# Kernel optimization log

Measured on AMD Instinct MI355X. Metric: run time of the kernel, lower is better.

Reference implementation:

```python
import jax, jax.numpy as jnp
import numpy as np

DIM = 128
R = 3
D = 2 * R + 1          # diameter = 7
D2 = D * D             # 49
B, H, W = 4, 64, 64
EPS_LN = 1e-6


def conv1x1(x, w, b):
    # x: [B,Cin,H,W], w: [Cout,Cin], b: [Cout]
    return jnp.einsum('oi,bihw->bohw', w, x) + b[None, :, None, None]


def ln2d(x, w, b):
    u = x.mean(1, keepdims=True)
    s = ((x - u) ** 2).mean(1, keepdims=True)
    xn = (x - u) / jnp.sqrt(s + EPS_LN)
    return w[None, :, None, None] * xn + b[None, :, None, None]


def extract_patches(x):
    # x: [B,C,H,W] -> [B,C,D2,H,W], n = ki*D+kj, value = padded[:, :, h+ki, w+kj]
    xp = jnp.pad(x, ((0, 0), (0, 0), (R, R), (R, R)), mode='reflect')
    Hh, Ww = x.shape[2], x.shape[3]
    return jnp.stack([xp[:, :, ki:ki + Hh, kj:kj + Ww]
                      for ki in range(D) for kj in range(D)], axis=2)


def setup_inputs() -> dict:
    key = jax.random.key(0)
    ks = jax.random.split(key, 16)
    sd = 0.02
    inp = {
        'spatial_feats': jax.random.normal(ks[0], (B, DIM, H, W), jnp.float32),
        'semantic_feats': jax.random.normal(ks[1], (B, DIM, H, W), jnp.float32),
        # range_proj: conv1x1 -> LN2d -> SiLU -> conv1x1
        'rp_w1': jax.random.normal(ks[2], (DIM, DIM), jnp.float32) * sd,
        'rp_b1': jnp.zeros((DIM,), jnp.float32),
        'rp_lnw': jnp.ones((DIM,), jnp.float32),
        'rp_lnb': jnp.zeros((DIM,), jnp.float32),
        'rp_w2': jax.random.normal(ks[3], (DIM, DIM), jnp.float32) * sd,
        'rp_b2': jnp.zeros((DIM,), jnp.float32),
        # fixup_proj: conv1x1(D2+DIM -> D2) -> LN2d -> SiLU -> conv1x1(D2 -> D2)
        'fx_w1': jax.random.normal(ks[4], (D2, D2 + DIM), jnp.float32) * sd,
        'fx_b1': jnp.zeros((D2,), jnp.float32),
        'fx_lnw': jnp.ones((D2,), jnp.float32),
        'fx_lnb': jnp.zeros((D2,), jnp.float32),
        'fx_w2': jax.random.normal(ks[5], (D2, D2), jnp.float32) * sd,
        'fx_b2': jnp.zeros((D2,), jnp.float32),
        'sigma_spatial': jnp.float32(1.0),
        # output_proj: conv1x1 -> LN2d -> conv1x1
        'op_w1': jax.random.normal(ks[6], (DIM, DIM), jnp.float32) * sd,
        'op_b1': jnp.zeros((DIM,), jnp.float32),
        'op_lnw': jnp.ones((DIM,), jnp.float32),
        'op_lnb': jnp.zeros((DIM,), jnp.float32),
        'op_w2': jax.random.normal(ks[7], (DIM, DIM), jnp.float32) * sd,
        'op_b2': jnp.zeros((DIM,), jnp.float32),
    }
    return inp


def reference(spatial_feats, semantic_feats,
              rp_w1, rp_b1, rp_lnw, rp_lnb, rp_w2, rp_b2,
              fx_w1, fx_b1, fx_lnw, fx_lnb, fx_w2, fx_b2,
              sigma_spatial,
              op_w1, op_b1, op_lnw, op_lnb, op_w2, op_b2):
    scale = DIM ** 0.5

    # range_proj (dropout is identity in eval)
    px = conv1x1(semantic_feats, rp_w1, rp_b1)
    px = jax.nn.silu(ln2d(px, rp_lnw, rp_lnb))
    proj_x = conv1x1(px, rp_w2, rp_b2)

    # spatial kernel [1, D2, 1, 1]
    dist = jnp.linspace(-1.0, 1.0, D)
    gx, gy = jnp.meshgrid(dist, dist, indexing='ij')
    spatial_kernel = jnp.exp(-(gx ** 2 + gy ** 2) /
                             (2.0 * sigma_spatial ** 2)).reshape(1, D2, 1, 1)

    # range kernel: softmax over neighborhood of <query, neighbor>/sqrt(dim)
    queries = extract_patches(proj_x)                    # [B,C,D2,H,W]
    sim = jnp.einsum('bcnhw,bchw->bnhw', queries, proj_x) / scale
    range_kernel = jax.nn.softmax(sim.astype(jnp.float32), axis=1)

    combined = range_kernel * spatial_kernel             # [B,D2,H,W]

    # fixup gating
    fx = conv1x1(jnp.concatenate([combined, semantic_feats], axis=1), fx_w1, fx_b1)
    fx = jax.nn.silu(ln2d(fx, fx_lnw, fx_lnb))
    fx = conv1x1(fx, fx_w2, fx_b2)
    combined = combined + combined * jax.nn.sigmoid(fx)
    combined = combined / (combined.sum(1, keepdims=True) + 1e-7)

    # weighted neighborhood aggregation of spatial features
    neighborhoods = extract_patches(spatial_feats)       # [B,C,D2,H,W]
    out = jnp.einsum('bcnhw,bnhw->bchw', neighborhoods, combined)

    # output_proj (no activation, dropout identity)
    out = conv1x1(out, op_w1, op_b1)
    out = ln2d(out, op_lnw, op_lnb)
    out = conv1x1(out, op_w2, op_b2)
    return out
```

## Files before the change

### kernel.cpp

```cpp
#include <hip/hip_runtime.h>
#include <cstdint>

#define BB 4
#define CDIM 128
#define HH 64
#define WW 64
#define RR 3
#define DD 7
#define DSQ 49

typedef __attribute__((ext_vector_type(8))) short short8v;
typedef __attribute__((ext_vector_type(4))) float float4v;

__device__ __forceinline__ int reflect64(int p) {
    p = (p < 0) ? -p : p;
    return (p > 63) ? (126 - p) : p;
}
__device__ __forceinline__ float sigm(float x) { return 1.0f / (1.0f + __expf(-x)); }
__device__ __forceinline__ short f2bf(float f) {
    uint32_t u = __float_as_uint(f);
    u += 0x7FFF + ((u >> 16) & 1);
    return (short)(u >> 16);
}

template<bool SILU>
__global__ __launch_bounds__(1024) void proj_kernel(
    const float* __restrict__ x, const float* __restrict__ w1,
    const float* __restrict__ b1, const float* __restrict__ lnw,
    const float* __restrict__ lnb, const float* __restrict__ w2,
    const float* __restrict__ b2, short* __restrict__ outT)
{
    __shared__ short sW1[CDIM * CDIM];
    __shared__ short sW2[CDIM * CDIM];
    __shared__ short sXT[WW * CDIM];
    __shared__ short sXT2[WW * CDIM];
    __shared__ float sT[CDIM][65];
    __shared__ float red1[16][WW];
    __shared__ float red2[16][WW];

    const int tid = threadIdx.x;
    const int l = tid & 63;
    const int q = tid >> 6;
    const int qu = __builtin_amdgcn_readfirstlane(q);
    const int b = blockIdx.x >> 6;
    const int h = blockIdx.x & 63;

    {
        const int o = tid >> 3;
        const int i0 = (tid & 7) * 16;
        const int sw = (o & 7) << 3;
        const float* wsrc[2] = {w1, w2};
        short* wdst[2] = {sW1, sW2};
        #pragma unroll
        for (int m = 0; m < 2; ++m) {
            const float* src = wsrc[m] + o * CDIM + i0;
            short8v pk0, pk1;
            #pragma unroll
            for (int j = 0; j < 8; ++j) pk0[j] = f2bf(src[j]);
            #pragma unroll
            for (int j = 0; j < 8; ++j) pk1[j] = f2bf(src[8 + j]);
            *reinterpret_cast<short8v*>(&wdst[m][o * 128 + (i0 ^ sw)]) = pk0;
            *reinterpret_cast<short8v*>(&wdst[m][o * 128 + ((i0 + 8) ^ sw)]) = pk1;
        }
    }
    {
        const int pos = tid & 15;
        const int c0 = tid >> 4;
        const float* xrow = x + (b * CDIM * HH + h) * WW;
        #pragma unroll
        for (int rr = 0; rr < 2; ++rr) {
            const int c = c0 + rr * 64;
            const float4 v = *reinterpret_cast<const float4*>(&xrow[c * HH * WW + pos * 4]);
            #pragma unroll
            for (int m = 0; m < 4; ++m) {
                const int p = pos * 4 + m;
                sXT[p * 128 + (c ^ ((p & 7) << 3))] = f2bf(((const float*)&v)[m]);
            }
        }
    }
    __syncthreads();

    const int lm = l & 15, g = l >> 4;
    const int tm = q >> 1;
    const int tn0 = (q & 1) * 2;
    const int oa = tm * 16 + lm;
    const int arow = oa * 128, asw = (oa & 7) << 3;
    const int p0 = tn0 * 16 + lm, p1 = (tn0 + 1) * 16 + lm;
    const int bsw0 = (p0 & 7) << 3, bsw1 = (p1 & 7) << 3;

    float4v acc0 = {0.f, 0.f, 0.f, 0.f}, acc1 = {0.f, 0.f, 0.f, 0.f};
    #pragma unroll
    for (int kk = 0; kk < 4; ++kk) {
        const int ki = kk * 32 + g * 8;
        const short8v af = *reinterpret_cast<const short8v*>(&sW1[arow + (ki ^ asw)]);
        const short8v bf0 = *reinterpret_cast<const short8v*>(&sXT[p0 * 128 + (ki ^ bsw0)]);
        const short8v bf1 = *reinterpret_cast<const short8v*>(&sXT[p1 * 128 + (ki ^ bsw1)]);
        acc0 = __builtin_amdgcn_mfma_f32_16x16x32_bf16(af, bf0, acc0, 0, 0, 0);
        acc1 = __builtin_amdgcn_mfma_f32_16x16x32_bf16(af, bf1, acc1, 0, 0, 0);
    }
    #pragma unroll
    for (int r = 0; r < 4; ++r) sT[tm * 16 + g * 4 + r][p0] = acc0[r];
    #pragma unroll
    for (int r = 0; r < 4; ++r) sT[tm * 16 + g * 4 + r][p1] = acc1[r];
    __syncthreads();

    {
        const int p = l;
        float vals[8];
        float s1 = 0.f, s2 = 0.f;
        #pragma unroll
        for (int j = 0; j < 8; ++j) {
            const float v = sT[qu * 8 + j][p] + b1[qu * 8 + j];
            vals[j] = v; s1 += v; s2 += v * v;
        }
        red1[q][p] = s1; red2[q][p] = s2;
        __syncthreads();
        float t1 = 0.f, t2 = 0.f;
        #pragma unroll
        for (int j = 0; j < 16; ++j) { t1 += red1[j][p]; t2 += red2[j][p]; }
        const float mean = t1 * (1.0f / 128.0f);
        const float var  = t2 * (1.0f / 128.0f) - mean * mean;
        const float rstd = rsqrtf(var + 1e-6f);
        short8v pk;
        #pragma unroll
        for (int j = 0; j < 8; ++j) {
            float v = (vals[j] - mean) * rstd * lnw[qu * 8 + j] + lnb[qu * 8 + j];
            if (SILU) v = v * sigm(v);
            pk[j] = f2bf(v);
        }
        *reinterpret_cast<short8v*>(&sXT2[p * 128 + ((qu * 8) ^ ((p & 7) << 3))]) = pk;
    }
    __syncthreads();

    {
        float4v a0 = {0.f, 0.f, 0.f, 0.f}, a1 = {0.f, 0.f, 0.f, 0.f};
        #pragma unroll
        for (int kk = 0; kk < 4; ++kk) {
            const int ki = kk * 32 + g * 8;
            const short8v af = *reinterpret_cast<const short8v*>(&sW2[arow + (ki ^ asw)]);
            const short8v bf0 = *reinterpret_cast<const short8v*>(&sXT2[p0 * 128 + (ki ^ bsw0)]);
            const short8v bf1 = *reinterpret_cast<const short8v*>(&sXT2[p1 * 128 + (ki ^ bsw1)]);
            a0 = __builtin_amdgcn_mfma_f32_16x16x32_bf16(af, bf0, a0, 0, 0, 0);
            a1 = __builtin_amdgcn_mfma_f32_16x16x32_bf16(af, bf1, a1, 0, 0, 0);
        }
        const float4 bv = *reinterpret_cast<const float4*>(&b2[tm * 16 + g * 4]);
        #pragma unroll
        for (int r = 0; r < 4; ++r) {
            const float bias = ((const float*)&bv)[r];
            sT[tm * 16 + g * 4 + r][p0] = a0[r] + bias;
            sT[tm * 16 + g * 4 + r][p1] = a1[r] + bias;
        }
    }
    __syncthreads();
    {
        const int p = tid >> 4;
        const int c0 = (tid & 15) * 8;
        short8v pk;
        #pragma unroll
        for (int j = 0; j < 8; ++j) pk[j] = f2bf(sT[c0 + j][p]);
        *reinterpret_cast<short8v*>(&outT[((b * HH + h) * WW + p) * CDIM + c0]) = pk;
    }
}

__global__ __launch_bounds__(1024) void simfixagg_kernel(
    const short* __restrict__ pxt, const float* __restrict__ sigma_p,
    const float* __restrict__ sem,
    const float* __restrict__ fw1, const float* __restrict__ fb1,
    const float* __restrict__ flnw, const float* __restrict__ flnb,
    const float* __restrict__ fw2, const float* __restrict__ fb2,
    const float* __restrict__ spatial,
    const float* __restrict__ ow1, const float* __restrict__ ob1,
    const float* __restrict__ olnw, const float* __restrict__ olnb,
    const float* __restrict__ ow2, const float* __restrict__ ob2,
    float* __restrict__ out)
{
    __shared__ alignas(16) char sBig[7 * WW * CDIM * 2];
    __shared__ alignas(16) char sAux[64 * 66 * 4];
    __shared__ alignas(16) float sSimWts[DSQ][64];
    __shared__ alignas(16) float sCmb[DSQ][66];

    short* rows = reinterpret_cast<short*>(sBig);
    short* B1   = reinterpret_cast<short*>(sBig);
    short* A1   = reinterpret_cast<short*>(sBig + 24576);
    short* B2   = reinterpret_cast<short*>(sBig + 49152);
    short* A2   = reinterpret_cast<short*>(sBig + 57344);
    float* fSem = reinterpret_cast<float*>(sBig + 65536);
    float* prm  = reinterpret_cast<float*>(sBig + 98304);
    short* W0   = reinterpret_cast<short*>(sBig);
    short* W1   = reinterpret_cast<short*>(sBig + 9216);
    short* sSa  = reinterpret_cast<short*>(sBig + 18432);
    float (*sT)[65] = reinterpret_cast<float(*)[65]>(sBig);
    short* sWb  = reinterpret_cast<short*>(sBig + 57344);
    short* sXT  = reinterpret_cast<short*>(sBig + 90112);

    float (*sP64)[66] = reinterpret_cast<float(*)[66]>(sAux);
    float (*red1)[65] = reinterpret_cast<float(*)[65]>(sAux);
    float (*red2)[65] = reinterpret_cast<float(*)[65]>(sAux + 16 * 65 * 4);

    const int tid = threadIdx.x;
    const int l = tid & 63;
    const int q = tid >> 6;
    const int qu = __builtin_amdgcn_readfirstlane(q);
    const int lbid = ((blockIdx.x & 7) << 5) | (blockIdx.x >> 3);
    const int b = lbid >> 6;
    const int h = lbid & 63;

    for (int idx = tid; idx < 7 * WW * 16; idx += 1024) {
        const int cchunk = idx & 15;
        const int p = (idx >> 4) & 63;
        const int row = idx >> 10;
        const int hp = reflect64(h + row - RR);
        const short8v v = *reinterpret_cast<const short8v*>(
            &pxt[((b * HH + hp) * WW + p) * CDIM + cchunk * 8]);
        *reinterpret_cast<short8v*>(
            &rows[(row * WW + p) * CDIM + ((cchunk * 8) ^ ((p & 7) << 3))]) = v;
    }
    __syncthreads();

    const int lm = l & 15, g = l >> 4;
    const int tm = q >> 2, tn = q & 3;
    const int pa = tm * 16 + lm;
    const int pxb = tn * 16 + lm;
    const int abase = (3 * WW + pa) * CDIM, as_ = (pa & 7) << 3;
    const int bs_ = (pxb & 7) << 3;

    short8v afr[4];
    #pragma unroll
    for (int kk = 0; kk < 4; ++kk)
        afr[kk] = *reinterpret_cast<const short8v*>(
            &rows[abase + ((kk * 32 + g * 8) ^ as_)]);

    const float rscale = 0.088388347648318447f;
    for (int ki = 0; ki < 7; ++ki) {
        float4v acc = {0.f, 0.f, 0.f, 0.f};
        const int bbase = (ki * WW + pxb) * CDIM;
        #pragma unroll
        for (int kk = 0; kk < 4; ++kk) {
            const short8v bf = *reinterpret_cast<const short8v*>(
                &rows[bbase + ((kk * 32 + g * 8) ^ bs_)]);
            acc = __builtin_amdgcn_mfma_f32_16x16x32_bf16(afr[kk], bf, acc, 0, 0, 0);
        }
        #pragma unroll
        for (int r = 0; r < 4; ++r)
            sP64[tm * 16 + g * 4 + r][tn * 16 + lm] = acc[r];
        __syncthreads();
        if (tid < 448) {
            const int kj = tid >> 6, p = tid & 63;
            sSimWts[ki * 7 + kj][p] = sP64[p][reflect64(p + kj - RR)] * rscale;
        }
        __syncthreads();
    }

    for (int idx = tid; idx < 64 * 24; idx += 1024) {
        const int o = idx / 24;
        const int ch0 = (idx % 24) * 8;
        short8v pk;
        #pragma unroll
        for (int j = 0; j < 8; ++j) {
            const int c = ch0 + j;
            float v = 0.f;
            if (o < DSQ) {
                if (c < DSQ) v = fw1[o * 177 + c];
                else if (c >= 64) v = fw1[o * 177 + DSQ + (c - 64)];
            }
            pk[j] = f2bf(v);
        }
        *reinterpret_cast<short8v*>(&A1[o * 192 + (ch0 ^ ((o & 7) << 3))]) = pk;
    }
    for (int idx = tid; idx < 64 * 8; idx += 1024) {
        const int o = idx >> 3;
        const int ch0 = (idx & 7) * 8;
        short8v pk;
        #pragma unroll
        for (int j = 0; j < 8; ++j) {
            const int c = ch0 + j;
            pk[j] = (o < DSQ && c < DSQ) ? f2bf(fw2[o * DSQ + c]) : (short)0;
        }
        *reinterpret_cast<short8v*>(&A2[o * 64 + (ch0 ^ ((o & 7) << 3))]) = pk;
    }
    {
        const short8v z = {0, 0, 0, 0, 0, 0, 0, 0};
        for (int idx = tid; idx < 64 * 8; idx += 1024)
            *reinterpret_cast<short8v*>(&B2[idx * 8]) = z;
    }
    for (int idx = tid; idx < 64 * 15; idx += 1024) {
        const int p = idx / 15, c = DSQ + idx % 15;
        B1[p * 192 + (c ^ ((p & 7) << 3))] = 0;
    }
    for (int idx = tid; idx < 256; idx += 1024) {
        const int a = idx >> 6, i = idx & 63;
        float v = 0.f;
        if (i < DSQ) {
            if (a == 0) v = fb1[i];
            else if (a == 1) v = flnw[i];
            else if (a == 2) v = flnb[i];
            else v = fb2[i];
        }
        prm[a * 64 + i] = v;
    }
    {
        const float* srow = sem + (b * CDIM * HH + h) * WW;
        for (int idx = tid; idx < CDIM * 16; idx += 1024) {
            const int r = idx >> 4, pos = idx & 15;
            *reinterpret_cast<float4*>(&fSem[r * WW + pos * 4]) =
                *reinterpret_cast<const float4*>(&srow[r * HH * WW + pos * 4]);
        }
    }
    {
        float rv[DSQ];
        #pragma unroll
        for (int n = 0; n < DSQ; ++n) rv[n] = sSimWts[n][l];
        float m = -1e30f;
        #pragma unroll
        for (int n = 0; n < DSQ; ++n) m = fmaxf(m, rv[n]);
        float ssum = 0.f;
        #pragma unroll
        for (int n = 0; n < DSQ; ++n) ssum += __expf(rv[n] - m);
        const float inv = 1.0f / ssum;
        const float sigma = sigma_p[0];
        const float inv2s2 = 1.0f / (2.0f * sigma * sigma);
        const int swl = (l & 7) << 3;
        #pragma unroll
        for (int k = 0; k < 4; ++k) {
            const int n = q + 16 * k;
            if (n < DSQ) {
                const int ki = n / 7, kj = n % 7;
                const float dx = (float)(ki - 3) * (1.0f / 3.0f);
                const float dy = (float)(kj - 3) * (1.0f / 3.0f);
                const float sk = __expf(-(dx * dx + dy * dy) * inv2s2);
                const float cv = __expf(rv[n] - m) * inv * sk;
                sCmb[n][l] = cv;
                B1[l * 192 + (n ^ swl)] = f2bf(cv);
            }
        }
    }
    __syncthreads();
    {
        const int c0 = q * 8;
        short8v pk;
        #pragma unroll
        for (int j = 0; j < 8; ++j) pk[j] = f2bf(fSem[(c0 + j) * WW + l]);
        *reinterpret_cast<short8v*>(&B1[l * 192 + ((64 + c0) ^ ((l & 7) << 3))]) = pk;
    }
    __syncthreads();

    const int oA = tm * 16 + lm;
    const int aswz = (oA & 7) << 3;
    const int p = tn * 16 + lm;
    const int bswz = (p & 7) << 3;

    float4v facc = {0.f, 0.f, 0.f, 0.f};
    #pragma unroll
    for (int kk = 0; kk < 6; ++kk) {
        const int ki = kk * 32 + g * 8;
        const short8v af = *reinterpret_cast<const short8v*>(&A1[oA * 192 + (ki ^ aswz)]);
        const short8v bf = *reinterpret_cast<const short8v*>(&B1[p * 192 + (ki ^ bswz)]);
        facc = __builtin_amdgcn_mfma_f32_16x16x32_bf16(af, bf, facc, 0, 0, 0);
    }
    float vals[4];
    float s1 = 0.f, s2 = 0.f;
    #pragma unroll
    for (int r = 0; r < 4; ++r) {
        const int o = tm * 16 + g * 4 + r;
        const float v = facc[r] + prm[o];
        vals[r] = v;
        if (o < DSQ) { s1 += v; s2 += v * v; }
    }
    red1[tm * 4 + g][p] = s1;
    red2[tm * 4 + g][p] = s2;
    __syncthreads();
    float t1 = 0.f, t2 = 0.f;
    #pragma unroll
    for (int j = 0; j < 16; ++j) { t1 += red1[j][p]; t2 += red2[j][p]; }
    const float mean = t1 * (1.0f / 49.0f);
    const float var  = t2 * (1.0f / 49.0f) - mean * mean;
    const float rstd = rsqrtf(var + 1e-6f);
    #pragma unroll
    for (int r = 0; r < 4; ++r) {
        const int o = tm * 16 + g * 4 + r;
        if (o < DSQ) {
            const float v = (vals[r] - mean) * rstd * prm[64 + o] + prm[128 + o];
            const float sv = v * sigm(v);
            B2[p * 64 + (o ^ bswz)] = f2bf(sv);
        }
    }
    __syncthreads();

    float4v facc2 = {0.f, 0.f, 0.f, 0.f};
    #pragma unroll
    for (int kk = 0; kk < 2; ++kk) {
        const int ki = kk * 32 + g * 8;
        const short8v af = *reinterpret_cast<const short8v*>(&A2[oA * 64 + (ki ^ aswz)]);
        const short8v bf = *reinterpret_cast<const short8v*>(&B2[p * 64 + (ki ^ bswz)]);
        facc2 = __builtin_amdgcn_mfma_f32_16x16x32_bf16(af, bf, facc2, 0, 0, 0);
    }
    float c2v[4];
    float ps = 0.f;
    #pragma unroll
    for (int r = 0; r < 4; ++r) {
        const int o = tm * 16 + g * 4 + r;
        if (o < DSQ) {
            const float f = facc2[r] + prm[192 + o];
            c2v[r] = sCmb[o][p] * (1.0f + sigm(f));
            ps += c2v[r];
        } else c2v[r] = 0.f;
    }
    red1[tm * 4 + g][p] = ps;
    __syncthreads();
    float tot = 0.f;
    #pragma unroll
    for (int j = 0; j < 16; ++j) tot += red1[j][p];
    const float invt = 1.0f / (tot + 1e-7f);
    #pragma unroll
    for (int r = 0; r < 4; ++r) {
        const int o = tm * 16 + g * 4 + r;
        if (o < DSQ) sSimWts[o][p] = c2v[r] * invt;
    }
    __syncthreads();

    {
        const int o = tid >> 3;
        const int i0 = (tid & 7) * 16;
        const int sw = (o & 7) << 3;
        const float* src = ow1 + o * CDIM + i0;
        short8v pk0, pk1;
        #pragma unroll
        for (int j = 0; j < 8; ++j) pk0[j] = f2bf(src[j]);
        #pragma unroll
        for (int j = 0; j < 8; ++j) pk1[j] = f2bf(src[8 + j]);
        *reinterpret_cast<short8v*>(&sWb[o * 128 + (i0 ^ sw)]) = pk0;
        *reinterpret_cast<short8v*>(&sWb[o * 128 + ((i0 + 8) ^ sw)]) = pk1;
    }

    const float* sb = spatial + b * CDIM * HH * WW;
    float4 sreg[2];
    #define LD_SROW(KI)                                                          \
        { const int hp_ = reflect64(h + (KI) - RR);                              \
          _Pragma("unroll")                                                      \
          for (int j = 0; j < 2; ++j) {                                          \
              const int idx = tid * 2 + j;                                       \
              const int c = idx >> 4, pos = idx & 15;                            \
              sreg[j] = *reinterpret_cast<const float4*>(                        \
                  &sb[(c * HH + hp_) * WW + pos * 4]);                           \
          } }
    #define ST_SROW()                                                            \
        { _Pragma("unroll")                                                      \
          for (int j = 0; j < 2; ++j) {                                          \
              const int idx = tid * 2 + j;                                       \
              const int c = idx >> 4, pos = idx & 15;                            \
              const int sw_ = (c & 7) << 3;                                      \
              _Pragma("unroll")                                                  \
              for (int m = 0; m < 4; ++m)                                        \
                  sSa[c * 64 + ((pos * 4 + m) ^ sw_)] =                          \
                      f2bf(((const float*)&sreg[j])[m]);                         \
          } }
    #define ZERO_W(DST)                                                          \
        { const short8v z8 = {0,0,0,0,0,0,0,0};                                  \
          if (tid < 576) *reinterpret_cast<short8v*>(&(DST)[tid * 8]) = z8; }
    #define SCATTER_W(DST, KIN)                                                  \
        if (tid < 64) {                                                          \
            const int pp_ = tid;                                                 \
            const int s_ = (pp_ > 3) ? (pp_ - 3) : 0;                            \
            float col[7] = {0.f, 0.f, 0.f, 0.f, 0.f, 0.f, 0.f};                  \
            _Pragma("unroll")                                                    \
            for (int kj = 0; kj < 7; ++kj) {                                     \
                const int pr = reflect64(pp_ + kj - RR);                         \
                const float wv_ = sSimWts[(KIN) * 7 + kj][pp_];                  \
                const int id_ = pr - s_;                                         \
                _Pragma("unroll")                                                \
                for (int jj = 0; jj < 7; ++jj) if (id_ == jj) col[jj] += wv_;    \
            }                                                                    \
            _Pragma("unroll")                                                    \
            for (int jj = 0; jj < 7; ++jj) {                                     \
                const int pr = s_ + jj;                                          \
                if (pr < 64) (DST)[pp_ * 72 + pr] = f2bf(col[jj]);               \
            }                                                                    \
        }

    ZERO_W(W0);
    ZERO_W(W1);
    LD_SROW(0);
    __syncthreads();
    SCATTER_W(W0, 0);
    ST_SROW();
    __syncthreads();

    const int tmA = q >> 1;
    const int oaA = tmA * 16 + lm;
    const int arA = oaA * 64, aswA = (oaA & 7) << 3;
    const int pA0 = ((q & 1) * 2) * 16 + lm, pA1 = ((q & 1) * 2 + 1) * 16 + lm;

    float4v ag0 = {0.f, 0.f, 0.f, 0.f}, ag1 = {0.f, 0.f, 0.f, 0.f};
    for (int ki = 0; ki < 7; ++ki) {
        if (ki < 6) LD_SROW(ki + 1);
        const short* Wc = (ki & 1) ? W1 : W0;
        #pragma unroll
        for (int kk = 0; kk < 2; ++kk) {
            const int k0 = kk * 32 + g * 8;
            const short8v a8 = *reinterpret_cast<const short8v*>(&sSa[arA + (k0 ^ aswA)]);
            const short8v b80 = *reinterpret_cast<const short8v*>(&Wc[pA0 * 72 + k0]);
            const short8v b81 = *reinterpret_cast<const short8v*>(&Wc[pA1 * 72 + k0]);
            ag0 = __builtin_amdgcn_mfma_f32_16x16x32_bf16(a8, b80, ag0, 0, 0, 0);
            ag1 = __builtin_amdgcn_mfma_f32_16x16x32_bf16(a8, b81, ag1, 0, 0, 0);
        }
        if (ki < 6) { SCATTER_W(((ki & 1) ? W0 : W1), ki + 1); }
        __syncthreads();
        if (ki < 6) {
            ST_SROW();
            if (ki & 1) { ZERO_W(W1); } else { ZERO_W(W0); }
            __syncthreads();
        }
    }
    #undef LD_SROW
    #undef ST_SROW
    #undef ZERO_W
    #undef SCATTER_W

    {
        #pragma unroll
        for (int r = 0; r < 4; ++r) {
            const int c = tmA * 16 + g * 4 + r;
            sXT[pA0 * 128 + (c ^ ((pA0 & 7) << 3))] = f2bf(ag0[r]);
            sXT[pA1 * 128 + (c ^ ((pA1 & 7) << 3))] = f2bf(ag1[r]);
        }
    }
    __syncthreads();

    const int tmo = q >> 1;
    const int tn0 = (q & 1) * 2;
    const int oaop = tmo * 16 + lm;
    const int arow = oaop * 128, asw = (oaop & 7) << 3;
    const int p0 = tn0 * 16 + lm, p1 = (tn0 + 1) * 16 + lm;
    const int bsw0 = (p0 & 7) << 3, bsw1 = (p1 & 7) << 3;

    {
        float4v a0 = {0.f, 0.f, 0.f, 0.f}, a1 = {0.f, 0.f, 0.f, 0.f};
        #pragma unroll
        for (int kk = 0; kk < 4; ++kk) {
            const int ki = kk * 32 + g * 8;
            const short8v af = *reinterpret_cast<const short8v*>(&sWb[arow + (ki ^ asw)]);
            const short8v bf0 = *reinterpret_cast<const short8v*>(&sXT[p0 * 128 + (ki ^ bsw0)]);
            const short8v bf1 = *reinterpret_cast<const short8v*>(&sXT[p1 * 128 + (ki ^ bsw1)]);
            a0 = __builtin_amdgcn_mfma_f32_16x16x32_bf16(af, bf0, a0, 0, 0, 0);
            a1 = __builtin_amdgcn_mfma_f32_16x16x32_bf16(af, bf1, a1, 0, 0, 0);
        }
        __syncthreads();
        #pragma unroll
        for (int r = 0; r < 4; ++r) sT[tmo * 16 + g * 4 + r][p0] = a0[r];
        #pragma unroll
        for (int r = 0; r < 4; ++r) sT[tmo * 16 + g * 4 + r][p1] = a1[r];
    }
    __syncthreads();

    {
        const int o = tid >> 3;
        const int i0 = (tid & 7) * 16;
        const int sw = (o & 7) << 3;
        const float* src = ow2 + o * CDIM + i0;
        short8v pk0, pk1;
        #pragma unroll
        for (int j = 0; j < 8; ++j) pk0[j] = f2bf(src[j]);
        #pragma unroll
        for (int j = 0; j < 8; ++j) pk1[j] = f2bf(src[8 + j]);
        *reinterpret_cast<short8v*>(&sWb[o * 128 + (i0 ^ sw)]) = pk0;
        *reinterpret_cast<short8v*>(&sWb[o * 128 + ((i0 + 8) ^ sw)]) = pk1;
    }
    {
        float vals2[8];
        float u1 = 0.f, u2 = 0.f;
        #pragma unroll
        for (int j = 0; j < 8; ++j) {
            const float v = sT[qu * 8 + j][l] + ob1[qu * 8 + j];
            vals2[j] = v; u1 += v; u2 += v * v;
        }
        red1[q][l] = u1; red2[q][l] = u2;
        __syncthreads();
        float v1 = 0.f, v2 = 0.f;
        #pragma unroll
        for (int j = 0; j < 16; ++j) { v1 += red1[j][l]; v2 += red2[j][l]; }
        const float mn = v1 * (1.0f / 128.0f);
        const float vr = v2 * (1.0f / 128.0f) - mn * mn;
        const float rs = rsqrtf(vr + 1e-6f);
        short8v pk;
        #pragma unroll
        for (int j = 0; j < 8; ++j) {
            const float v = (vals2[j] - mn) * rs * olnw[qu * 8 + j] + olnb[qu * 8 + j];
            pk[j] = f2bf(v);
        }
        *reinterpret_cast<short8v*>(&sXT[l * 128 + ((qu * 8) ^ ((l & 7) << 3))]) = pk;
    }
    __syncthreads();

    {
        float4v a0 = {0.f, 0.f, 0.f, 0.f}, a1 = {0.f, 0.f, 0.f, 0.f};
        #pragma unroll
        for (int kk = 0; kk < 4; ++kk) {
            const int ki = kk * 32 + g * 8;
            const short8v af = *reinterpret_cast<const short8v*>(&sWb[arow + (ki ^ asw)]);
            const short8v bf0 = *reinterpret_cast<const short8v*>(&sXT[p0 * 128 + (ki ^ bsw0)]);
            const short8v bf1 = *reinterpret_cast<const short8v*>(&sXT[p1 * 128 + (ki ^ bsw1)]);
            a0 = __builtin_amdgcn_mfma_f32_16x16x32_bf16(af, bf0, a0, 0, 0, 0);
            a1 = __builtin_amdgcn_mfma_f32_16x16x32_bf16(af, bf1, a1, 0, 0, 0);
        }
        const float4 bv = *reinterpret_cast<const float4*>(&ob2[tmo * 16 + g * 4]);
        float* obase = out + (b * CDIM * HH + h) * WW;
        #pragma unroll
        for (int r = 0; r < 4; ++r) {
            const float bias = ((const float*)&bv)[r];
            obase[(tmo * 16 + g * 4 + r) * HH * WW + p0] = a0[r] + bias;
            obase[(tmo * 16 + g * 4 + r) * HH * WW + p1] = a1[r] + bias;
        }
    }
}

extern "C" void kernel_launch(void* const* d_in, const int* in_sizes, int n_in,
                              void* d_out, int out_size, void* d_ws, size_t ws_size,
                              hipStream_t stream) {
    (void)in_sizes; (void)n_in; (void)out_size; (void)ws_size;
    const float* spatial  = (const float*)d_in[0];
    const float* semantic = (const float*)d_in[1];
    const float* rp_w1 = (const float*)d_in[2];
    const float* rp_b1 = (const float*)d_in[3];
    const float* rp_lnw = (const float*)d_in[4];
    const float* rp_lnb = (const float*)d_in[5];
    const float* rp_w2 = (const float*)d_in[6];
    const float* rp_b2 = (const float*)d_in[7];
    const float* fx_w1 = (const float*)d_in[8];
    const float* fx_b1 = (const float*)d_in[9];
    const float* fx_lnw = (const float*)d_in[10];
    const float* fx_lnb = (const float*)d_in[11];
    const float* fx_w2 = (const float*)d_in[12];
    const float* fx_b2 = (const float*)d_in[13];
    const float* sigma = (const float*)d_in[14];
    const float* op_w1 = (const float*)d_in[15];
    const float* op_b1 = (const float*)d_in[16];
    const float* op_lnw = (const float*)d_in[17];
    const float* op_lnb = (const float*)d_in[18];
    const float* op_w2 = (const float*)d_in[19];
    const float* op_b2 = (const float*)d_in[20];

    char* wsb = (char*)d_ws;
    short* pxt  = (short*)wsb;
    float* outp = (float*)d_out;

    dim3 grid(BB * HH), blk(1024);
    proj_kernel<true><<<grid, blk, 0, stream>>>(semantic, rp_w1, rp_b1, rp_lnw, rp_lnb,
                                                rp_w2, rp_b2, pxt);
    simfixagg_kernel<<<grid, blk, 0, stream>>>(pxt, sigma, semantic,
                                               fx_w1, fx_b1, fx_lnw, fx_lnb, fx_w2, fx_b2,
                                               spatial,
                                               op_w1, op_b1, op_lnw, op_lnb, op_w2, op_b2,
                                               outp);
}
```

Before: 54.43 us.

## Precompute all seven aggregation weight rows and double-buffer spatial rows

Builds all seven banded weight matrices at once with 448 threads before the aggregation loop, instead of scattering one per iteration with 64 threads. Spatial rows are double-buffered so each loop iteration needs one barrier instead of two. Row stores become vectorised 4-short writes. The output-projection weight load moves after the aggregation to free shared memory. This costs more shared-memory layout pressure and adds one up-front step where 448 threads zero and fill the weight rows.

```diff
diff --git a/kernel.cpp b/kernel.cpp
--- a/kernel.cpp
+++ b/kernel.cpp
@@ -10,6 +10,7 @@
 #define DSQ 49
 
 typedef __attribute__((ext_vector_type(8))) short short8v;
+typedef __attribute__((ext_vector_type(4))) short short4v;
 typedef __attribute__((ext_vector_type(4))) float float4v;
 
 __device__ __forceinline__ int reflect64(int p) {
@@ -186,12 +187,12 @@
     short* A2   = reinterpret_cast<short*>(sBig + 57344);
     float* fSem = reinterpret_cast<float*>(sBig + 65536);
     float* prm  = reinterpret_cast<float*>(sBig + 98304);
-    short* W0   = reinterpret_cast<short*>(sBig);
-    short* W1   = reinterpret_cast<short*>(sBig + 9216);
-    short* sSa  = reinterpret_cast<short*>(sBig + 18432);
-    float (*sT)[65] = reinterpret_cast<float(*)[65]>(sBig);
-    short* sWb  = reinterpret_cast<short*>(sBig + 57344);
-    short* sXT  = reinterpret_cast<short*>(sBig + 90112);
+    short* W7   = reinterpret_cast<short*>(sBig);
+    short* sSa0 = reinterpret_cast<short*>(sBig + 64512);
+    short* sSa1 = reinterpret_cast<short*>(sBig + 80896);
+    short* sWb  = reinterpret_cast<short*>(sBig);
+    short* sXT  = reinterpret_cast<short*>(sBig + 32768);
+    float (*sT)[65] = reinterpret_cast<float(*)[65]>(sBig + 49152);
 
     float (*sP64)[66] = reinterpret_cast<float(*)[66]>(sAux);
     float (*red1)[65] = reinterpret_cast<float(*)[65]>(sAux);
@@ -418,20 +419,6 @@
     }
     __syncthreads();
 
-    {
-        const int o = tid >> 3;
-        const int i0 = (tid & 7) * 16;
-        const int sw = (o & 7) << 3;
-        const float* src = ow1 + o * CDIM + i0;
-        short8v pk0, pk1;
-        #pragma unroll
-        for (int j = 0; j < 8; ++j) pk0[j] = f2bf(src[j]);
-        #pragma unroll
-        for (int j = 0; j < 8; ++j) pk1[j] = f2bf(src[8 + j]);
-        *reinterpret_cast<short8v*>(&sWb[o * 128 + (i0 ^ sw)]) = pk0;
-        *reinterpret_cast<short8v*>(&sWb[o * 128 + ((i0 + 8) ^ sw)]) = pk1;
-    }
-
     const float* sb = spatial + b * CDIM * HH * WW;
     float4 sreg[2];
     #define LD_SROW(KI)                                                          \
@@ -443,46 +430,43 @@
               sreg[j] = *reinterpret_cast<const float4*>(                        \
                   &sb[(c * HH + hp_) * WW + pos * 4]);                           \
           } }
-    #define ST_SROW()                                                            \
+    #define ST_SROW(DST)                                                         \
         { _Pragma("unroll")                                                      \
           for (int j = 0; j < 2; ++j) {                                          \
               const int idx = tid * 2 + j;                                       \
               const int c = idx >> 4, pos = idx & 15;                            \
               const int sw_ = (c & 7) << 3;                                      \
+              short4v pk;                                                        \
               _Pragma("unroll")                                                  \
-              for (int m = 0; m < 4; ++m)                                        \
-                  sSa[c * 64 + ((pos * 4 + m) ^ sw_)] =                          \
-                      f2bf(((const float*)&sreg[j])[m]);                         \
+              for (int m = 0; m < 4; ++m) pk[m] = f2bf(((const float*)&sreg[j])[m]); \
+              *reinterpret_cast<short4v*>(&(DST)[c * 64 + ((pos * 4) ^ sw_)]) = pk;  \
           } }
-    #define ZERO_W(DST)                                                          \
-        { const short8v z8 = {0,0,0,0,0,0,0,0};                                  \
-          if (tid < 576) *reinterpret_cast<short8v*>(&(DST)[tid * 8]) = z8; }
-    #define SCATTER_W(DST, KIN)                                                  \
-        if (tid < 64) {                                                          \
-            const int pp_ = tid;                                                 \
-            const int s_ = (pp_ > 3) ? (pp_ - 3) : 0;                            \
-            float col[7] = {0.f, 0.f, 0.f, 0.f, 0.f, 0.f, 0.f};                  \
-            _Pragma("unroll")                                                    \
-            for (int kj = 0; kj < 7; ++kj) {                                     \
-                const int pr = reflect64(pp_ + kj - RR);                         \
-                const float wv_ = sSimWts[(KIN) * 7 + kj][pp_];                  \
-                const int id_ = pr - s_;                                         \
-                _Pragma("unroll")                                                \
-                for (int jj = 0; jj < 7; ++jj) if (id_ == jj) col[jj] += wv_;    \
-            }                                                                    \
-            _Pragma("unroll")                                                    \
-            for (int jj = 0; jj < 7; ++jj) {                                     \
-                const int pr = s_ + jj;                                          \
-                if (pr < 64) (DST)[pp_ * 72 + pr] = f2bf(col[jj]);               \
-            }                                                                    \
-        }
-
-    ZERO_W(W0);
-    ZERO_W(W1);
+
     LD_SROW(0);
-    __syncthreads();
-    SCATTER_W(W0, 0);
-    ST_SROW();
+    if (tid < 448) {
+        const int kin = tid >> 6, pp_ = tid & 63;
+        const int s_ = (pp_ > 3) ? (pp_ - 3) : 0;
+        float col[7] = {0.f, 0.f, 0.f, 0.f, 0.f, 0.f, 0.f};
+        #pragma unroll
+        for (int kj = 0; kj < 7; ++kj) {
+            const int pr = reflect64(pp_ + kj - RR);
+            const float wv_ = sSimWts[kin * 7 + kj][pp_];
+            const int id_ = pr - s_;
+            #pragma unroll
+            for (int jj = 0; jj < 7; ++jj) if (id_ == jj) col[jj] += wv_;
+        }
+        short* wrow = &W7[(kin * 64 + pp_) * 72];
+        const short8v z8 = {0, 0, 0, 0, 0, 0, 0, 0};
+        #pragma unroll
+        for (int j8 = 0; j8 < 9; ++j8)
+            *reinterpret_cast<short8v*>(&wrow[j8 * 8]) = z8;
+        #pragma unroll
+        for (int jj = 0; jj < 7; ++jj) {
+            const int pr = s_ + jj;
+            if (pr < 64) wrow[pr] = f2bf(col[jj]);
+        }
+    }
+    ST_SROW(sSa0);
     __syncthreads();
 
     const int tmA = q >> 1;
@@ -493,28 +477,22 @@
     float4v ag0 = {0.f, 0.f, 0.f, 0.f}, ag1 = {0.f, 0.f, 0.f, 0.f};
     for (int ki = 0; ki < 7; ++ki) {
         if (ki < 6) LD_SROW(ki + 1);
-        const short* Wc = (ki & 1) ? W1 : W0;
+        const short* Sc = (ki & 1) ? sSa1 : sSa0;
+        const short* Wc = &W7[ki * 64 * 72];
         #pragma unroll
         for (int kk = 0; kk < 2; ++kk) {
             const int k0 = kk * 32 + g * 8;
-            const short8v a8 = *reinterpret_cast<const short8v*>(&sSa[arA + (k0 ^ aswA)]);
+            const short8v a8 = *reinterpret_cast<const short8v*>(&Sc[arA + (k0 ^ aswA)]);
             const short8v b80 = *reinterpret_cast<const short8v*>(&Wc[pA0 * 72 + k0]);
             const short8v b81 = *reinterpret_cast<const short8v*>(&Wc[pA1 * 72 + k0]);
             ag0 = __builtin_amdgcn_mfma_f32_16x16x32_bf16(a8, b80, ag0, 0, 0, 0);
             ag1 = __builtin_amdgcn_mfma_f32_16x16x32_bf16(a8, b81, ag1, 0, 0, 0);
         }
-        if (ki < 6) { SCATTER_W(((ki & 1) ? W0 : W1), ki + 1); }
+        if (ki < 6) { ST_SROW(((ki & 1) ? sSa0 : sSa1)); }
         __syncthreads();
-        if (ki < 6) {
-            ST_SROW();
-            if (ki & 1) { ZERO_W(W1); } else { ZERO_W(W0); }
-            __syncthreads();
-        }
     }
     #undef LD_SROW
     #undef ST_SROW
-    #undef ZERO_W
-    #undef SCATTER_W
 
     {
         #pragma unroll
@@ -523,6 +501,19 @@
             sXT[pA0 * 128 + (c ^ ((pA0 & 7) << 3))] = f2bf(ag0[r]);
             sXT[pA1 * 128 + (c ^ ((pA1 & 7) << 3))] = f2bf(ag1[r]);
         }
+    }
+    {
+        const int o = tid >> 3;
+        const int i0 = (tid & 7) * 16;
+        const int sw = (o & 7) << 3;
+        const float* src = ow1 + o * CDIM + i0;
+        short8v pk0, pk1;
+        #pragma unroll
+        for (int j = 0; j < 8; ++j) pk0[j] = f2bf(src[j]);
+        #pragma unroll
+        for (int j = 0; j < 8; ++j) pk1[j] = f2bf(src[8 + j]);
+        *reinterpret_cast<short8v*>(&sWb[o * 128 + (i0 ^ sw)]) = pk0;
+        *reinterpret_cast<short8v*>(&sWb[o * 128 + ((i0 + 8) ^ sw)]) = pk1;
     }
     __syncthreads();
 
```

Result: faster. 48.84 us (-10.3%).
